# Kernel tuning notes

Hardware: AMD Instinct MI355X
Metric: run time of the kernel (lower is better)

Reference implementation:

```python
import jax, jax.numpy as jnp
import numpy as np

ALPHA = 2.0
BIG = 1e9

def _edt(feat):
    # Exact Euclidean distance from every pixel to the nearest True pixel in feat [H,W].
    # Separable algorithm: exact 1D pass along rows (axis 0), then min-plus with
    # squared column offsets (Felzenszwalb-style lower envelope, done brute force).
    H, W = feat.shape
    pos = jnp.arange(H, dtype=jnp.float32)[:, None]            # [H,1]
    last = jax.lax.cummax(jnp.where(feat, pos, -BIG), axis=0)  # nearest feature above (incl.)
    nxt = -jax.lax.cummax(jnp.where(feat, -pos, -BIG), axis=0, reverse=True)
    g = jnp.minimum(pos - last, nxt - pos)                     # [H,W] 1D distance per column
    g = jnp.minimum(g, jnp.float32(H + W))                     # cap columns with no feature
    j = jnp.arange(W, dtype=jnp.float32)
    cross = (j[:, None] - j[None, :]) ** 2                     # [W,W] (y - w)^2
    # D[h,y] = min_w g[h,w]^2 + (y-w)^2
    D = jnp.min(g[:, None, :] ** 2 + cross[None, :, :], axis=-1)
    return jnp.sqrt(D)

def _dist_map(mask):
    # scipy: fg_dist = edt(mask==0 input) -> distance to nearest mask==1 pixel;
    #        bg_dist = edt(mask==1 input) -> distance to nearest mask==0 pixel.
    return _edt(mask == 1.0) + _edt(mask == 0.0)

def setup_inputs() -> dict:
    key = jax.random.key(0)
    k1, k2 = jax.random.split(key)
    B, H, W = 32, 256, 256
    pred = jax.random.uniform(k1, (B, 1, H, W), dtype=jnp.float32)
    target = (jax.random.uniform(k2, (B, 1, H, W)) < 0.5).astype(jnp.float32)
    return {"pred": pred, "target": target}

def reference(pred, target):
    pred_bin = (pred > 0.5).astype(jnp.float32)
    # sequential over batch to bound the [H,W,W] min-plus intermediate
    pred_dist = jax.lax.map(_dist_map, pred_bin[:, 0])   # [B,H,W]
    target_dist = jax.lax.map(_dist_map, target[:, 0])   # [B,H,W]
    dist_diff = (pred_dist - target_dist) ** 2
    weighted = dist_diff * target_dist ** ALPHA
    return jnp.mean(weighted)
```

## Files before the change

### kernel.cpp

```cpp
#include <hip/hip_runtime.h>
#include <math.h>

#define HH 256
#define WW 256
#define BB 32
#define NW 8

__global__ __launch_bounds__(256) void bitmask_kernel(
    const float* __restrict__ pred, const float* __restrict__ tgt,
    unsigned int* __restrict__ P, unsigned int* __restrict__ T) {
  const int b  = blockIdx.x >> 5;
  const int j  = (blockIdx.x >> 2) & 7;
  const int wq = blockIdx.x & 3;
  const int r    = threadIdx.x >> 6;
  const int lane = threadIdx.x & 63;
  const int col  = wq * 64 + lane;
  const int row0 = j * 32 + r * 8;

  const float* pin = pred + (size_t)b * (HH * WW) + row0 * WW + col;
  const float* tin = tgt  + (size_t)b * (HH * WW) + row0 * WW + col;
  unsigned int pb = 0, tb = 0;
#pragma unroll
  for (int i = 0; i < 8; ++i) {
    pb |= (pin[i * WW] > 0.5f ? 1u : 0u) << i;
    tb |= (tin[i * WW] == 1.0f ? 1u : 0u) << i;
  }

  __shared__ unsigned int sP[4][64], sT[4][64];
  sP[r][lane] = pb << (r * 8);
  sT[r][lane] = tb << (r * 8);
  __syncthreads();
  if (r == 0) {
    P[((size_t)b * NW + j) * WW + col] =
        sP[0][lane] | sP[1][lane] | sP[2][lane] | sP[3][lane];
    T[((size_t)b * NW + j) * WW + col] =
        sT[0][lane] | sT[1][lane] | sT[2][lane] | sT[3][lane];
  }
}

__global__ __launch_bounds__(512) void stripe_kernel(
    const unsigned int* __restrict__ P, const unsigned int* __restrict__ T,
    float* __restrict__ partial) {
  const int blk = blockIdx.x;
  const int b = blk >> 3;
  const int j = blk & 7;
  const int tid = threadIdx.x;

  __shared__ float sp[32][WW];
  __shared__ float st[32][WW];

  {
    const int mp = tid >> 8;
    const int w  = tid & 255;
    const unsigned int* M = mp ? T : P;

    unsigned int Wd[NW];
#pragma unroll
    for (int jj = 0; jj < NW; ++jj)
      Wd[jj] = M[((size_t)b * NW + jj) * WW + w];

    unsigned int E[NW];
#pragma unroll
    for (int jj = 0; jj < NW - 1; ++jj)
      E[jj] = Wd[jj] ^ ((Wd[jj] >> 1) | (Wd[jj + 1] << 31));
    E[NW - 1] = (Wd[NW - 1] ^ (Wd[NW - 1] >> 1)) & 0x7FFFFFFFu;

    unsigned int EJ = 0, EJm1 = 0, WJ = 0;
#pragma unroll
    for (int jj = 0; jj < NW; ++jj) {
      if (j == jj) { EJ = E[jj]; WJ = Wd[jj]; }
      if (j - 1 == jj) EJm1 = E[jj];
    }

    int emax = -100000;
#pragma unroll
    for (int jj = 0; jj < NW - 1; ++jj)
      if (jj < j && E[jj]) emax = 32 * jj + 31 - __builtin_clz(E[jj]);
    int D = (j * 32 - 1) - emax;
    if (D > 513) D = 513;

    int emin = 100000;
#pragma unroll
    for (int jj = NW - 1; jj >= 1; --jj)
      if (jj > j && E[jj]) emin = 32 * jj + __builtin_ctz(E[jj]);
    int U = (emin + 1) - (j * 32 + 32);
    if (U > 513) U = 513;

    const unsigned int EQ = (EJ << 1) | (j ? (EJm1 >> 31) : 0u);

    unsigned int dn[16];
#pragma unroll
    for (int i = 0; i < 32; ++i) {
      D = ((EQ >> i) & 1u) ? 1 : (D + 1);
      if (i & 1) dn[i >> 1] |= (unsigned int)D << 16;
      else       dn[i >> 1] = (unsigned int)D;
    }

#pragma unroll
    for (int i = 31; i >= 0; --i) {
      U = ((EJ >> i) & 1u) ? 1 : (U + 1);
      int dnv = (int)((dn[i >> 1] >> ((i & 1) * 16)) & 0xFFFFu);
      int g = min(min(dnv, U), 512);
      float g2 = (float)(g * g);
      float v = ((WJ >> i) & 1u) ? -g2 : g2;
      if (mp == 0) sp[i][w] = v;
      else         st[i][w] = v;
    }
  }
  __syncthreads();

  const int wv = tid >> 6;
  const int lane = tid & 63;
  float acc = 0.f;

  for (int rr = 0; rr < 4; ++rr) {
    const int r = wv * 4 + rr;
    float m[4][4];
#pragma unroll
    for (int c = 0; c < 4; ++c) {
      float vp = sp[r][lane + 64 * c];
      float vt = st[r][lane + 64 * c];
      m[c][0] = fmaxf(vp, 0.f); m[c][1] = fmaxf(-vp, 0.f);
      m[c][2] = fmaxf(vt, 0.f); m[c][3] = fmaxf(-vt, 0.f);
    }

    for (int k = 1; k < WW; ++k) {
      const float c2 = (float)(k * k);
      float mx = 0.f;
#pragma unroll
      for (int c = 0; c < 4; ++c)
        mx = fmaxf(mx, fmaxf(fmaxf(m[c][0], m[c][1]), fmaxf(m[c][2], m[c][3])));
      if (c2 >= mx) break;
#pragma unroll
      for (int c = 0; c < 4; ++c) {
        const int y = lane + 64 * c;
        const int lo = y - k;
        if (lo >= 0) {
          float vp = sp[r][lo], vt = st[r][lo];
          m[c][0] = fminf(m[c][0], fmaxf(vp, 0.f) + c2);
          m[c][1] = fminf(m[c][1], fmaxf(-vp, 0.f) + c2);
          m[c][2] = fminf(m[c][2], fmaxf(vt, 0.f) + c2);
          m[c][3] = fminf(m[c][3], fmaxf(-vt, 0.f) + c2);
        }
        const int hi = y + k;
        if (hi < WW) {
          float vp = sp[r][hi], vt = st[r][hi];
          m[c][0] = fminf(m[c][0], fmaxf(vp, 0.f) + c2);
          m[c][1] = fminf(m[c][1], fmaxf(-vp, 0.f) + c2);
          m[c][2] = fminf(m[c][2], fmaxf(vt, 0.f) + c2);
          m[c][3] = fminf(m[c][3], fmaxf(-vt, 0.f) + c2);
        }
      }
    }

    float val = 0.f;
#pragma unroll
    for (int c = 0; c < 4; ++c) {
      float pd = sqrtf(m[c][0]) + sqrtf(m[c][1]);
      float td = sqrtf(m[c][2]) + sqrtf(m[c][3]);
      float diff = pd - td;
      val += diff * diff * td * td;
    }
    for (int off = 32; off > 0; off >>= 1) val += __shfl_down(val, off);
    acc += val;
  }

  if (lane == 0) partial[blk * 8 + wv] = acc;
}

__global__ __launch_bounds__(256) void finalize_kernel(
    const float* __restrict__ partial, float* __restrict__ out) {
  __shared__ double sd[256];
  double sum = 0.0;
  for (int i = threadIdx.x; i < 2048; i += 256) sum += (double)partial[i];
  sd[threadIdx.x] = sum;
  __syncthreads();
  for (int stride = 128; stride > 0; stride >>= 1) {
    if (threadIdx.x < stride) sd[threadIdx.x] += sd[threadIdx.x + stride];
    __syncthreads();
  }
  if (threadIdx.x == 0)
    out[0] = (float)(sd[0] / (double)((size_t)BB * HH * WW));
}

extern "C" void kernel_launch(void* const* d_in, const int* in_sizes, int n_in,
                              void* d_out, int out_size, void* d_ws, size_t ws_size,
                              hipStream_t stream) {
  const float* pred = (const float*)d_in[0];
  const float* tgt  = (const float*)d_in[1];
  float* out = (float*)d_out;

  unsigned int* P = (unsigned int*)d_ws;
  unsigned int* T = P + (size_t)BB * NW * WW;
  float* partial = (float*)(T + (size_t)BB * NW * WW);

  hipLaunchKernelGGL(bitmask_kernel, dim3(BB * NW * 4), dim3(256), 0, stream,
                     pred, tgt, P, T);
  hipLaunchKernelGGL(stripe_kernel, dim3(BB * NW), dim3(512), 0, stream,
                     P, T, partial);
  hipLaunchKernelGGL(finalize_kernel, dim3(1), dim3(256), 0, stream,
                     partial, out);
}
```

Before: 28.82 us.

## Split stripes into 8-row blocks and pack pred/target distances as float4

Each block now handles 8 rows instead of 32, so the grid grows fourfold and each wave processes a single row rather than looping over four. The 1D column distances for pred and target are stored already split into positive and negative parts in a float4 shared array, so the min-plus inner loop needs one vector LDS read and no fmax per neighbor. The cost is redundant recomputation of column bitmask scans per block and a larger partial buffer for the finalize reduction.

```diff
diff --git a/kernel.cpp b/kernel.cpp
--- a/kernel.cpp
+++ b/kernel.cpp
@@ -38,16 +38,17 @@
   }
 }
 
-__global__ __launch_bounds__(512) void stripe_kernel(
+__global__ __launch_bounds__(512) void stripe8_kernel(
     const unsigned int* __restrict__ P, const unsigned int* __restrict__ T,
     float* __restrict__ partial) {
   const int blk = blockIdx.x;
-  const int b = blk >> 3;
-  const int j = blk & 7;
+  const int b  = blk >> 5;
+  const int js = blk & 31;
+  const int base = js * 8;
+  const int wq0 = base >> 5, sub = base & 31;
   const int tid = threadIdx.x;
 
-  __shared__ float sp[32][WW];
-  __shared__ float st[32][WW];
+  __shared__ float4 sv[8][WW];
 
   {
     const int mp = tid >> 8;
@@ -65,114 +66,113 @@
       E[jj] = Wd[jj] ^ ((Wd[jj] >> 1) | (Wd[jj + 1] << 31));
     E[NW - 1] = (Wd[NW - 1] ^ (Wd[NW - 1] >> 1)) & 0x7FFFFFFFu;
 
-    unsigned int EJ = 0, EJm1 = 0, WJ = 0;
+    unsigned int Ew = 0, Ewm1 = 0, Ww = 0;
 #pragma unroll
     for (int jj = 0; jj < NW; ++jj) {
-      if (j == jj) { EJ = E[jj]; WJ = Wd[jj]; }
-      if (j - 1 == jj) EJm1 = E[jj];
-    }
-
+      if (jj == wq0) { Ew = E[jj]; Ww = Wd[jj]; }
+      if (jj == wq0 - 1) Ewm1 = E[jj];
+    }
+    const unsigned int EU8 = (Ew >> sub) & 0xFFu;
+    const unsigned int EQ8 =
+        sub ? ((Ew >> (sub - 1)) & 0xFFu)
+            : (((Ew << 1) | (wq0 ? (Ewm1 >> 31) : 0u)) & 0xFFu);
+    const unsigned int W8 = (Ww >> sub) & 0xFFu;
+
+    const unsigned int submask = sub ? ((1u << sub) - 1u) : 0u;
     int emax = -100000;
 #pragma unroll
-    for (int jj = 0; jj < NW - 1; ++jj)
-      if (jj < j && E[jj]) emax = 32 * jj + 31 - __builtin_clz(E[jj]);
-    int D = (j * 32 - 1) - emax;
+    for (int jj = 0; jj < NW; ++jj) {
+      unsigned int a = (jj < wq0) ? E[jj]
+                                  : ((jj == wq0) ? (E[jj] & submask) : 0u);
+      if (a) emax = 32 * jj + 31 - __builtin_clz(a);
+    }
+    int D = (base - 1) - emax;
     if (D > 513) D = 513;
 
+    const int r8 = base + 8;
+    const int wr = r8 >> 5;
+    const unsigned int upmask =
+        (r8 & 31) ? ~((1u << (r8 & 31)) - 1u) : 0xFFFFFFFFu;
     int emin = 100000;
 #pragma unroll
-    for (int jj = NW - 1; jj >= 1; --jj)
-      if (jj > j && E[jj]) emin = 32 * jj + __builtin_ctz(E[jj]);
-    int U = (emin + 1) - (j * 32 + 32);
+    for (int jj = NW - 1; jj >= 0; --jj) {
+      unsigned int a = (jj > wr) ? E[jj]
+                                 : ((jj == wr) ? (E[jj] & upmask) : 0u);
+      if (a) emin = 32 * jj + __builtin_ctz(a);
+    }
+    int U = (emin + 1) - r8;
     if (U > 513) U = 513;
 
-    const unsigned int EQ = (EJ << 1) | (j ? (EJm1 >> 31) : 0u);
-
-    unsigned int dn[16];
-#pragma unroll
-    for (int i = 0; i < 32; ++i) {
-      D = ((EQ >> i) & 1u) ? 1 : (D + 1);
-      if (i & 1) dn[i >> 1] |= (unsigned int)D << 16;
-      else       dn[i >> 1] = (unsigned int)D;
-    }
-
-#pragma unroll
-    for (int i = 31; i >= 0; --i) {
-      U = ((EJ >> i) & 1u) ? 1 : (U + 1);
-      int dnv = (int)((dn[i >> 1] >> ((i & 1) * 16)) & 0xFFFFu);
-      int g = min(min(dnv, U), 512);
+    int dn[8];
+#pragma unroll
+    for (int i = 0; i < 8; ++i) {
+      D = ((EQ8 >> i) & 1u) ? 1 : (D + 1);
+      dn[i] = D;
+    }
+#pragma unroll
+    for (int i = 7; i >= 0; --i) {
+      U = ((EU8 >> i) & 1u) ? 1 : (U + 1);
+      int g = min(min(dn[i], U), 512);
       float g2 = (float)(g * g);
-      float v = ((WJ >> i) & 1u) ? -g2 : g2;
-      if (mp == 0) sp[i][w] = v;
-      else         st[i][w] = v;
+      bool own = (W8 >> i) & 1u;
+      float2 v = own ? make_float2(0.f, g2) : make_float2(g2, 0.f);
+      *(((float2*)&sv[i][w]) + mp) = v;
     }
   }
   __syncthreads();
 
   const int wv = tid >> 6;
   const int lane = tid & 63;
-  float acc = 0.f;
-
-  for (int rr = 0; rr < 4; ++rr) {
-    const int r = wv * 4 + rr;
-    float m[4][4];
+
+  float m[4][4];
+#pragma unroll
+  for (int c = 0; c < 4; ++c) {
+    float4 v = sv[wv][lane + 64 * c];
+    m[c][0] = v.x; m[c][1] = v.y; m[c][2] = v.z; m[c][3] = v.w;
+  }
+
+  for (int k = 1; k < WW; ++k) {
+    const float c2 = (float)(k * k);
+    float mx = 0.f;
+#pragma unroll
+    for (int c = 0; c < 4; ++c)
+      mx = fmaxf(mx, fmaxf(fmaxf(m[c][0], m[c][1]), fmaxf(m[c][2], m[c][3])));
+    if (c2 >= mx) break;
 #pragma unroll
     for (int c = 0; c < 4; ++c) {
-      float vp = sp[r][lane + 64 * c];
-      float vt = st[r][lane + 64 * c];
-      m[c][0] = fmaxf(vp, 0.f); m[c][1] = fmaxf(-vp, 0.f);
-      m[c][2] = fmaxf(vt, 0.f); m[c][3] = fmaxf(-vt, 0.f);
-    }
-
-    for (int k = 1; k < WW; ++k) {
-      const float c2 = (float)(k * k);
-      float mx = 0.f;
-#pragma unroll
-      for (int c = 0; c < 4; ++c)
-        mx = fmaxf(mx, fmaxf(fmaxf(m[c][0], m[c][1]), fmaxf(m[c][2], m[c][3])));
-      if (c2 >= mx) break;
-#pragma unroll
-      for (int c = 0; c < 4; ++c) {
-        const int y = lane + 64 * c;
-        const int lo = y - k;
-        if (lo >= 0) {
-          float vp = sp[r][lo], vt = st[r][lo];
-          m[c][0] = fminf(m[c][0], fmaxf(vp, 0.f) + c2);
-          m[c][1] = fminf(m[c][1], fmaxf(-vp, 0.f) + c2);
-          m[c][2] = fminf(m[c][2], fmaxf(vt, 0.f) + c2);
-          m[c][3] = fminf(m[c][3], fmaxf(-vt, 0.f) + c2);
-        }
-        const int hi = y + k;
-        if (hi < WW) {
-          float vp = sp[r][hi], vt = st[r][hi];
-          m[c][0] = fminf(m[c][0], fmaxf(vp, 0.f) + c2);
-          m[c][1] = fminf(m[c][1], fmaxf(-vp, 0.f) + c2);
-          m[c][2] = fminf(m[c][2], fmaxf(vt, 0.f) + c2);
-          m[c][3] = fminf(m[c][3], fmaxf(-vt, 0.f) + c2);
-        }
+      const int y = lane + 64 * c;
+      const int lo = y - k;
+      if (lo >= 0) {
+        float4 v = sv[wv][lo];
+        m[c][0] = fminf(m[c][0], v.x + c2); m[c][1] = fminf(m[c][1], v.y + c2);
+        m[c][2] = fminf(m[c][2], v.z + c2); m[c][3] = fminf(m[c][3], v.w + c2);
       }
-    }
-
-    float val = 0.f;
-#pragma unroll
-    for (int c = 0; c < 4; ++c) {
-      float pd = sqrtf(m[c][0]) + sqrtf(m[c][1]);
-      float td = sqrtf(m[c][2]) + sqrtf(m[c][3]);
-      float diff = pd - td;
-      val += diff * diff * td * td;
-    }
-    for (int off = 32; off > 0; off >>= 1) val += __shfl_down(val, off);
-    acc += val;
-  }
-
-  if (lane == 0) partial[blk * 8 + wv] = acc;
+      const int hi = y + k;
+      if (hi < WW) {
+        float4 v = sv[wv][hi];
+        m[c][0] = fminf(m[c][0], v.x + c2); m[c][1] = fminf(m[c][1], v.y + c2);
+        m[c][2] = fminf(m[c][2], v.z + c2); m[c][3] = fminf(m[c][3], v.w + c2);
+      }
+    }
+  }
+
+  float val = 0.f;
+#pragma unroll
+  for (int c = 0; c < 4; ++c) {
+    float pd = sqrtf(m[c][0]) + sqrtf(m[c][1]);
+    float td = sqrtf(m[c][2]) + sqrtf(m[c][3]);
+    float diff = pd - td;
+    val += diff * diff * td * td;
+  }
+  for (int off = 32; off > 0; off >>= 1) val += __shfl_down(val, off);
+  if (lane == 0) partial[blk * 8 + wv] = val;
 }
 
 __global__ __launch_bounds__(256) void finalize_kernel(
     const float* __restrict__ partial, float* __restrict__ out) {
   __shared__ double sd[256];
   double sum = 0.0;
-  for (int i = threadIdx.x; i < 2048; i += 256) sum += (double)partial[i];
+  for (int i = threadIdx.x; i < BB * HH; i += 256) sum += (double)partial[i];
   sd[threadIdx.x] = sum;
   __syncthreads();
   for (int stride = 128; stride > 0; stride >>= 1) {
@@ -196,7 +196,7 @@
 
   hipLaunchKernelGGL(bitmask_kernel, dim3(BB * NW * 4), dim3(256), 0, stream,
                      pred, tgt, P, T);
-  hipLaunchKernelGGL(stripe_kernel, dim3(BB * NW), dim3(512), 0, stream,
+  hipLaunchKernelGGL(stripe8_kernel, dim3(BB * 32), dim3(512), 0, stream,
                      P, T, partial);
   hipLaunchKernelGGL(finalize_kernel, dim3(1), dim3(256), 0, stream,
                      partial, out);
```

Result: slower. 30.46 us (+5.7%).

## Merge the two per-pixel EDT min-plus chains by sign and fuse finalize

Applied to the files above, without the earlier changes.

Each pixel's foreground and background distances have one term that is always zero. The min-plus pass therefore keeps one accumulator per map instead of two, using a per-pixel sign mask to select which neighbours count. The pred and target stripe values are interleaved as float2 so one shared-memory load serves both. The separate finalize kernel is removed: the last block, detected with an atomic counter that the bitmask kernel resets, does the final reduction. This adds inter-kernel atomic ordering and a more intricate sign-based correctness argument.

```diff
diff --git a/kernel.cpp b/kernel.cpp
--- a/kernel.cpp
+++ b/kernel.cpp
@@ -8,7 +8,11 @@
 
 __global__ __launch_bounds__(256) void bitmask_kernel(
     const float* __restrict__ pred, const float* __restrict__ tgt,
-    unsigned int* __restrict__ P, unsigned int* __restrict__ T) {
+    unsigned int* __restrict__ P, unsigned int* __restrict__ T,
+    unsigned int* __restrict__ cnt) {
+  if (blockIdx.x == 0 && threadIdx.x == 0)
+    __hip_atomic_store(cnt, 0u, __ATOMIC_RELAXED, __HIP_MEMORY_SCOPE_AGENT);
+
   const int b  = blockIdx.x >> 5;
   const int j  = (blockIdx.x >> 2) & 7;
   const int wq = blockIdx.x & 3;
@@ -40,14 +44,16 @@
 
 __global__ __launch_bounds__(512) void stripe_kernel(
     const unsigned int* __restrict__ P, const unsigned int* __restrict__ T,
-    float* __restrict__ partial) {
+    float* __restrict__ partial, unsigned int* __restrict__ cnt,
+    float* __restrict__ out) {
   const int blk = blockIdx.x;
   const int b = blk >> 3;
   const int j = blk & 7;
   const int tid = threadIdx.x;
 
-  __shared__ float sp[32][WW];
-  __shared__ float st[32][WW];
+  __shared__ float2 sv[32][WW];
+  __shared__ double sd[512];
+  __shared__ unsigned int isLast;
 
   {
     const int mp = tid >> 8;
@@ -103,8 +109,7 @@
       int g = min(min(dnv, U), 512);
       float g2 = (float)(g * g);
       float v = ((WJ >> i) & 1u) ? -g2 : g2;
-      if (mp == 0) sp[i][w] = v;
-      else         st[i][w] = v;
+      *(((float*)&sv[i][w]) + mp) = v;
     }
   }
   __syncthreads();
@@ -115,72 +120,80 @@
 
   for (int rr = 0; rr < 4; ++rr) {
     const int r = wv * 4 + rr;
-    float m[4][4];
+
+    float m1[4], m2[4];
+    unsigned int sg1[4], sg2[4];
 #pragma unroll
     for (int c = 0; c < 4; ++c) {
-      float vp = sp[r][lane + 64 * c];
-      float vt = st[r][lane + 64 * c];
-      m[c][0] = fmaxf(vp, 0.f); m[c][1] = fmaxf(-vp, 0.f);
-      m[c][2] = fmaxf(vt, 0.f); m[c][3] = fmaxf(-vt, 0.f);
+      float2 v = sv[r][lane + 64 * c];
+      sg1[c] = __float_as_uint(v.x) & 0x80000000u;
+      sg2[c] = __float_as_uint(v.y) & 0x80000000u;
+      m1[c] = fabsf(v.x);
+      m2[c] = fabsf(v.y);
     }
 
     for (int k = 1; k < WW; ++k) {
       const float c2 = (float)(k * k);
-      float mx = 0.f;
-#pragma unroll
-      for (int c = 0; c < 4; ++c)
-        mx = fmaxf(mx, fmaxf(fmaxf(m[c][0], m[c][1]), fmaxf(m[c][2], m[c][3])));
+      float mx = fmaxf(fmaxf(fmaxf(m1[0], m1[1]), fmaxf(m1[2], m1[3])),
+                       fmaxf(fmaxf(m2[0], m2[1]), fmaxf(m2[2], m2[3])));
       if (c2 >= mx) break;
 #pragma unroll
       for (int c = 0; c < 4; ++c) {
         const int y = lane + 64 * c;
         const int lo = y - k;
         if (lo >= 0) {
-          float vp = sp[r][lo], vt = st[r][lo];
-          m[c][0] = fminf(m[c][0], fmaxf(vp, 0.f) + c2);
-          m[c][1] = fminf(m[c][1], fmaxf(-vp, 0.f) + c2);
-          m[c][2] = fminf(m[c][2], fmaxf(vt, 0.f) + c2);
-          m[c][3] = fminf(m[c][3], fmaxf(-vt, 0.f) + c2);
+          float2 v = sv[r][lo];
+          m1[c] = fminf(m1[c],
+              fmaxf(__uint_as_float(__float_as_uint(v.x) ^ sg1[c]), 0.f) + c2);
+          m2[c] = fminf(m2[c],
+              fmaxf(__uint_as_float(__float_as_uint(v.y) ^ sg2[c]), 0.f) + c2);
         }
         const int hi = y + k;
         if (hi < WW) {
-          float vp = sp[r][hi], vt = st[r][hi];
-          m[c][0] = fminf(m[c][0], fmaxf(vp, 0.f) + c2);
-          m[c][1] = fminf(m[c][1], fmaxf(-vp, 0.f) + c2);
-          m[c][2] = fminf(m[c][2], fmaxf(vt, 0.f) + c2);
-          m[c][3] = fminf(m[c][3], fmaxf(-vt, 0.f) + c2);
+          float2 v = sv[r][hi];
+          m1[c] = fminf(m1[c],
+              fmaxf(__uint_as_float(__float_as_uint(v.x) ^ sg1[c]), 0.f) + c2);
+          m2[c] = fminf(m2[c],
+              fmaxf(__uint_as_float(__float_as_uint(v.y) ^ sg2[c]), 0.f) + c2);
         }
       }
     }
 
-    float val = 0.f;
 #pragma unroll
     for (int c = 0; c < 4; ++c) {
-      float pd = sqrtf(m[c][0]) + sqrtf(m[c][1]);
-      float td = sqrtf(m[c][2]) + sqrtf(m[c][3]);
+      float pd = sqrtf(m1[c]);
+      float td = sqrtf(m2[c]);
       float diff = pd - td;
-      val += diff * diff * td * td;
-    }
-    for (int off = 32; off > 0; off >>= 1) val += __shfl_down(val, off);
-    acc += val;
-  }
-
-  if (lane == 0) partial[blk * 8 + wv] = acc;
-}
-
-__global__ __launch_bounds__(256) void finalize_kernel(
-    const float* __restrict__ partial, float* __restrict__ out) {
-  __shared__ double sd[256];
-  double sum = 0.0;
-  for (int i = threadIdx.x; i < 2048; i += 256) sum += (double)partial[i];
-  sd[threadIdx.x] = sum;
-  __syncthreads();
-  for (int stride = 128; stride > 0; stride >>= 1) {
-    if (threadIdx.x < stride) sd[threadIdx.x] += sd[threadIdx.x + stride];
+      acc += diff * diff * (td * td);
+    }
+  }
+
+  for (int off = 32; off > 0; off >>= 1) acc += __shfl_down(acc, off);
+  if (lane == 0)
+    __hip_atomic_store(&partial[blk * 8 + wv], acc, __ATOMIC_RELAXED,
+                       __HIP_MEMORY_SCOPE_AGENT);
+
+  __syncthreads();
+  if (tid == 0) {
+    unsigned int old = __hip_atomic_fetch_add(cnt, 1u, __ATOMIC_ACQ_REL,
+                                              __HIP_MEMORY_SCOPE_AGENT);
+    isLast = (old == (unsigned int)(BB * NW - 1)) ? 1u : 0u;
+  }
+  __syncthreads();
+  if (isLast) {
+    double s = 0.0;
+    for (int i = tid; i < BB * NW * 8; i += 512)
+      s += (double)__hip_atomic_load(&partial[i], __ATOMIC_RELAXED,
+                                     __HIP_MEMORY_SCOPE_AGENT);
+    sd[tid] = s;
     __syncthreads();
-  }
-  if (threadIdx.x == 0)
-    out[0] = (float)(sd[0] / (double)((size_t)BB * HH * WW));
+    for (int st = 256; st > 0; st >>= 1) {
+      if (tid < st) sd[tid] += sd[tid + st];
+      __syncthreads();
+    }
+    if (tid == 0)
+      out[0] = (float)(sd[0] / (double)((size_t)BB * HH * WW));
+  }
 }
 
 extern "C" void kernel_launch(void* const* d_in, const int* in_sizes, int n_in,
@@ -193,11 +206,10 @@
   unsigned int* P = (unsigned int*)d_ws;
   unsigned int* T = P + (size_t)BB * NW * WW;
   float* partial = (float*)(T + (size_t)BB * NW * WW);
+  unsigned int* cnt = (unsigned int*)(partial + BB * NW * 8);
 
   hipLaunchKernelGGL(bitmask_kernel, dim3(BB * NW * 4), dim3(256), 0, stream,
-                     pred, tgt, P, T);
+                     pred, tgt, P, T, cnt);
   hipLaunchKernelGGL(stripe_kernel, dim3(BB * NW), dim3(512), 0, stream,
-                     P, T, partial);
-  hipLaunchKernelGGL(finalize_kernel, dim3(1), dim3(256), 0, stream,
-                     partial, out);
+                     P, T, partial, cnt, out);
 }
```

After: 25.74 us. 1.12x faster.
